# Kernel optimization log

Measured on AMD Instinct MI355X. Metric: run time of the kernel, lower is better.

## Reference

```python
import jax, jax.numpy as jnp
import numpy as np

N, E, D, S, H, L = 20000, 320000, 128, 16, 4, 64


def _ln(x, g, b):
    m = x.mean(-1, keepdims=True)
    v = jnp.mean((x - m) ** 2, -1, keepdims=True)
    return (x - m) / jnp.sqrt(v + 1e-6) * g + b


def _mlp3(x, w1, b1, g1, be1, w2, b2, g2, be2, w3, b3):
    h = jax.nn.silu(_ln(x @ w1 + b1, g1, be1))
    h = jax.nn.silu(_ln(h @ w2 + b2, g2, be2))
    return h @ w3 + b3


def _seg_softmax(a, idx, n):
    # torch_geometric.utils.softmax: per-destination-group stable softmax
    m = jax.ops.segment_max(a, idx, num_segments=n)
    m = jnp.where(jnp.isfinite(m), m, 0.0)
    e = jnp.exp(a - m[idx])
    s = jax.ops.segment_sum(e, idx, num_segments=n)
    return e / (s[idx] + 1e-16)


def setup_inputs() -> dict:
    key = jax.random.key(0)
    ks = jax.random.split(key, 32)
    rn = lambda k, sh, sc=1.0: jax.random.normal(k, sh, dtype=jnp.float32) * sc
    li = lambda k, fi, fo: rn(k, (fi, fo), 1.0 / np.sqrt(fi))
    z = lambda n_: jnp.zeros((n_,), jnp.float32)
    o = lambda n_: jnp.ones((n_,), jnp.float32)
    inp = {
        'node_in': rn(ks[0], (N, D)),
        'node_embed': rn(ks[1], (N, D)),
        'edge_sh': rn(ks[2], (E, S)),
        'edge_length_embedding': rn(ks[3], (E, L)),
        'edge_src': jax.random.randint(ks[4], (E,), 0, N, dtype=jnp.int32),
        'edge_dst': jax.random.randint(ks[5], (E,), 0, N, dtype=jnp.int32),
        'batch': jnp.zeros((N,), jnp.int32),
        'pre_lin_w': li(ks[6], 2 * D + L, D),
        'tp2_w1': li(ks[7], L, 64), 'tp2_b1': z(64),
        'tp2_w2': li(ks[8], 64, H * S), 'tp2_b2': z(H * S),
        'a_w1': li(ks[9], L, 64), 'a_b1': z(64), 'a_g1': o(64), 'a_be1': z(64),
        'a_w2': li(ks[10], 64, 64), 'a_b2': z(64), 'a_g2': o(64), 'a_be2': z(64),
        'a_w3': li(ks[11], 64, H), 'a_b3': z(H),
        'lin_w': li(ks[12], D * H, D),
        'lin_edge_w': li(ks[13], D * H, 64),
        's_w1': li(ks[14], 64, 64), 's_b1': z(64), 's_g1': o(64), 's_be1': z(64),
        's_w2': li(ks[15], 64, 64), 's_b2': z(64), 's_g2': o(64), 's_be2': z(64),
        's_w3': li(ks[16], 64, 32), 's_b3': z(32),
    }
    return inp


def reference(node_in, node_embed, edge_sh, edge_length_embedding, edge_src, edge_dst, batch,
              pre_lin_w, tp2_w1, tp2_b1, tp2_w2, tp2_b2,
              a_w1, a_b1, a_g1, a_be1, a_w2, a_b2, a_g2, a_be2, a_w3, a_b3,
              lin_w, lin_edge_w,
              s_w1, s_b1, s_g1, s_be1, s_w2, s_b2, s_g2, s_be2, s_w3, s_b3):
    e = edge_length_embedding.shape[0]
    n = node_in.shape[0]
    # gather + pre_lin
    msg = jnp.concatenate([node_in[edge_src], node_in[edge_dst], edge_length_embedding], -1) @ pre_lin_w  # [E,D]
    # EquiConv tp2: channelwise TP with radial-MLP per-edge per-(head,sh) weights
    radial = jax.nn.silu(edge_length_embedding @ tp2_w1 + tp2_b1) @ tp2_w2 + tp2_b2  # [E,H*S]
    scal = jnp.einsum('ehs,es->eh', radial.reshape(e, H, S), edge_sh)  # [E,H]
    value = msg[:, None, :] * scal[:, :, None]  # [E,H,D]
    alpha = _mlp3(edge_length_embedding, a_w1, a_b1, a_g1, a_be1, a_w2, a_b2, a_g2, a_be2, a_w3, a_b3)  # [E,H]
    edge_out = value * alpha[:, :, None]  # [E,H,D]
    edge_scalar = _mlp3(edge_out.reshape(e, -1) @ lin_edge_w,
                        s_w1, s_b1, s_g1, s_be1, s_w2, s_b2, s_g2, s_be2, s_w3, s_b3)  # [E,32]
    asm = _seg_softmax(alpha, edge_dst, n)  # [E,H]
    node_fea = jax.ops.segment_sum(value * asm[:, :, None], edge_dst, num_segments=n)  # [N,H,D]
    node_out = node_fea.reshape(n, -1) @ lin_w  # [N,D]
    return node_out, edge_scalar
```

## Files before the change

### kernel.cpp

```cpp
#include <hip/hip_runtime.h>

#define NN 20000
#define EE 320000
#define WTOT 27648

typedef unsigned short u16;
typedef unsigned int u32;
typedef __attribute__((ext_vector_type(8))) short bf16x8;
typedef __attribute__((ext_vector_type(8))) _Float16 f16x8;
typedef __attribute__((ext_vector_type(4))) float f32x4;

__device__ __forceinline__ float bf2f(u16 u){
  union { u32 i; float f; } v; v.i = ((u32)u) << 16; return v.f;
}
__device__ __forceinline__ u16 f2bf(float f){
  union { float f; u32 i; } v; v.f = f;
  u32 i = v.i;
  return (u16)((i + 0x7FFFu + ((i >> 16) & 1u)) >> 16);
}
__device__ __forceinline__ u16 f2h(float f){
  union { _Float16 h[2]; u32 u; } v; v.h[0] = (_Float16)f;
  return (u16)(v.u & 0xFFFF);
}
__device__ __forceinline__ float h2f(u16 u){
  union { u32 i; _Float16 h[2]; } v; v.i = u; return (float)v.h[0];
}
__device__ __forceinline__ u32 packh2(float a, float b){
  return ((u32)f2h(b) << 16) | (u32)f2h(a);
}

__global__ __launch_bounds__(256) void k_prep(
    const float* __restrict__ plw, const float* __restrict__ lew,
    const float* __restrict__ lw,
    u16* __restrict__ Bt1, u16* __restrict__ Bt2, u16* __restrict__ Bt3)
{
  int i = blockIdx.x * 256 + threadIdx.x;
  if (i < 128*320) {
    int n = i / 320, k = i % 320;
    Bt1[i] = f2h(plw[k*128 + n]);
  }
  int j = i - 128*320;
  if (j >= 0 && j < 256*128) {
    int n = j / 128, k = j % 128;
    int h = n >> 6, c = n & 63;
    Bt2[j] = f2h(lew[(h*128 + k)*64 + c]);
  }
  int l = i - 128*320 - 256*128;
  if (l >= 0 && l < 128*512) {
    int n = l / 512, k = l % 512;
    Bt3[l] = f2bf(lw[k*128 + n]);
  }
}

__global__ __launch_bounds__(256) void k_prep2(
    const float* __restrict__ aw1, const float* __restrict__ aw2, const float* __restrict__ aw3,
    const float* __restrict__ rw1, const float* __restrict__ rw2,
    const float* __restrict__ sw1, const float* __restrict__ sw2, const float* __restrict__ sw3,
    u16* __restrict__ W)
{
  int i = blockIdx.x * 256 + threadIdx.x;
  if (i >= WTOT) return;
  float v = 0.f;
  int j = i;
  if (j < 8192)      { int n = j >> 6, k = j & 63;
                       v = (n < 64) ? aw1[k*64 + n] : rw1[k*64 + (n - 64)]; }
  else if ((j -= 8192) < 4096) { int n = j >> 6, k = j & 63; v = aw2[k*64 + n]; }
  else if ((j -= 4096) < 1024) { int n = j >> 6, k = j & 63; v = (n < 4) ? aw3[k*4 + n] : 0.f; }
  else if ((j -= 1024) < 4096) { int n = j >> 6, k = j & 63; v = rw2[k*64 + n]; }
  else if ((j -= 4096) < 4096) { int n = j >> 6, k = j & 63; v = sw1[k*64 + n]; }
  else if ((j -= 4096) < 4096) { int n = j >> 6, k = j & 63; v = sw2[k*64 + n]; }
  else               { j -= 4096; int n = j >> 6, k = j & 63; v = sw3[k*32 + n]; }
  W[i] = f2h(v);
}

__global__ __launch_bounds__(256) void k_prep3(
    const float* __restrict__ elen, const float* __restrict__ node_in,
    u16* __restrict__ elen16, u16* __restrict__ node16)
{
  size_t i = (size_t)blockIdx.x * 256 + threadIdx.x;
  const size_t n1 = (size_t)EE * 64 / 8;
  const float* src;
  u16* dst;
  if (i < n1) { src = elen + i*8; dst = elen16 + i*8; }
  else {
    size_t j = i - n1;
    if (j >= (size_t)NN * 128 / 8) return;
    src = node_in + j*8; dst = node16 + j*8;
  }
  float4 a = ((const float4*)src)[0];
  float4 b = ((const float4*)src)[1];
  uint4 vh;
  vh.x = packh2(a.x, a.y); vh.y = packh2(a.z, a.w);
  vh.z = packh2(b.x, b.y); vh.w = packh2(b.z, b.w);
  *(uint4*)dst = vh;
}

__global__ __launch_bounds__(256) void k_zero(int* __restrict__ counts){
  int i = blockIdx.x * 256 + threadIdx.x;
  if (i < NN) counts[i] = 0;
}
__global__ __launch_bounds__(256) void k_count(const int* __restrict__ edst, int* __restrict__ counts){
  int e = blockIdx.x * 256 + threadIdx.x;
  if (e < EE) atomicAdd(&counts[edst[e]], 1);
}
__global__ __launch_bounds__(1024) void k_scan(const int* __restrict__ counts,
                                               int* __restrict__ offs, int* __restrict__ cursor){
  __shared__ int part[1024];
  int t = threadIdx.x;
  int c0 = t * 20, c1 = c0 + 20; if (c1 > NN) c1 = NN; if (c0 > NN) c0 = NN;
  int s = 0;
  for (int i = c0; i < c1; ++i) s += counts[i];
  part[t] = s;
  __syncthreads();
  if (t == 0) {
    int run = 0;
    for (int i = 0; i < 1024; ++i) { int v = part[i]; part[i] = run; run += v; }
    offs[NN] = run;
  }
  __syncthreads();
  int run = part[t];
  for (int i = c0; i < c1; ++i) { offs[i] = run; cursor[i] = run; run += counts[i]; }
}
__global__ __launch_bounds__(256) void k_fill(const int* __restrict__ edst,
                                              int* __restrict__ cursor, int* __restrict__ eids){
  int e = blockIdx.x * 256 + threadIdx.x;
  if (e < EE) { int p = atomicAdd(&cursor[edst[e]], 1); eids[p] = e; }
}
__global__ __launch_bounds__(256) void k_sort(const int* __restrict__ offs, int* __restrict__ eids){
  int n = blockIdx.x * 256 + threadIdx.x;
  if (n >= NN) return;
  int b = offs[n], e = offs[n+1];
  for (int i = b + 1; i < e; ++i) {
    int v = eids[i]; int j = i - 1;
    while (j >= b && eids[j] > v) { eids[j+1] = eids[j]; --j; }
    eids[j+1] = v;
  }
}

template<int NI>
__device__ __forceinline__ void gemm16_lds(const u16 (*X)[72], int wrow, int lane,
                                           const u16* __restrict__ B, f32x4 acc[2][4])
{
  const int fr = lane & 15, fc = lane >> 4;
  #pragma unroll
  for (int mi = 0; mi < 2; ++mi)
    #pragma unroll
    for (int ni = 0; ni < NI; ++ni)
      acc[mi][ni] = (f32x4){0.f, 0.f, 0.f, 0.f};
  #pragma unroll
  for (int kk = 0; kk < 2; ++kk) {
    f16x8 a0 = *(const f16x8*)&X[wrow + fr][kk*32 + fc*8];
    f16x8 a1 = *(const f16x8*)&X[wrow + 16 + fr][kk*32 + fc*8];
    #pragma unroll
    for (int ni = 0; ni < NI; ++ni) {
      f16x8 b = *(const f16x8*)(B + (size_t)(ni*16 + fr)*64 + kk*32 + fc*8);
      acc[0][ni] = __builtin_amdgcn_mfma_f32_16x16x32_f16(a0, b, acc[0][ni], 0, 0, 0);
      acc[1][ni] = __builtin_amdgcn_mfma_f32_16x16x32_f16(a1, b, acc[1][ni], 0, 0, 0);
    }
  }
}

template<int NI>
__device__ __forceinline__ void gemm16_lds1(const u16 (*X)[72], int wrow, int lane,
                                            const u16* __restrict__ B, f32x4 acc[4])
{
  const int fr = lane & 15, fc = lane >> 4;
  #pragma unroll
  for (int ni = 0; ni < NI; ++ni) acc[ni] = (f32x4){0.f, 0.f, 0.f, 0.f};
  #pragma unroll
  for (int kk = 0; kk < 2; ++kk) {
    f16x8 a = *(const f16x8*)&X[wrow + fr][kk*32 + fc*8];
    #pragma unroll
    for (int ni = 0; ni < NI; ++ni) {
      f16x8 b = *(const f16x8*)(B + (size_t)(ni*16 + fr)*64 + kk*32 + fc*8);
      acc[ni] = __builtin_amdgcn_mfma_f32_16x16x32_f16(a, b, acc[ni], 0, 0, 0);
    }
  }
}

__device__ __forceinline__ void gemm16_glb8(const u16* __restrict__ X, int row0, int lane,
                                            const u16* __restrict__ B, f32x4 acc[2][8])
{
  const int fr = lane & 15, fc = lane >> 4;
  #pragma unroll
  for (int mi = 0; mi < 2; ++mi)
    #pragma unroll
    for (int ni = 0; ni < 8; ++ni)
      acc[mi][ni] = (f32x4){0.f, 0.f, 0.f, 0.f};
  #pragma unroll
  for (int kk = 0; kk < 2; ++kk) {
    f16x8 a0 = *(const f16x8*)(X + (size_t)(row0 + fr)*64 + kk*32 + fc*8);
    f16x8 a1 = *(const f16x8*)(X + (size_t)(row0 + 16 + fr)*64 + kk*32 + fc*8);
    #pragma unroll
    for (int ni = 0; ni < 8; ++ni) {
      f16x8 b = *(const f16x8*)(B + (size_t)(ni*16 + fr)*64 + kk*32 + fc*8);
      acc[0][ni] = __builtin_amdgcn_mfma_f32_16x16x32_f16(a0, b, acc[0][ni], 0, 0, 0);
      acc[1][ni] = __builtin_amdgcn_mfma_f32_16x16x32_f16(a1, b, acc[1][ni], 0, 0, 0);
    }
  }
}

template<bool LN>
__device__ __forceinline__ void act_store16(f32x4 acc[2][4],
    const float* __restrict__ b, const float* __restrict__ g, const float* __restrict__ be,
    u16 (*H)[72], int wrow, int lane)
{
  const int fr = lane & 15, fc = lane >> 4;
  float bv[4], gv[4], bev[4];
  #pragma unroll
  for (int ni = 0; ni < 4; ++ni) {
    bv[ni] = b[ni*16 + fr];
    if (LN) { gv[ni] = g[ni*16 + fr]; bev[ni] = be[ni*16 + fr]; }
  }
  #pragma unroll
  for (int mi = 0; mi < 2; ++mi)
    #pragma unroll
    for (int j = 0; j < 4; ++j) {
      int r = wrow + mi*16 + fc*4 + j;
      float x[4];
      #pragma unroll
      for (int ni = 0; ni < 4; ++ni) x[ni] = acc[mi][ni][j] + bv[ni];
      if (LN) {
        float s  = x[0] + x[1] + x[2] + x[3];
        float s2 = x[0]*x[0] + x[1]*x[1] + x[2]*x[2] + x[3]*x[3];
        #pragma unroll
        for (int off = 1; off < 16; off <<= 1) {
          s  += __shfl_xor(s,  off);
          s2 += __shfl_xor(s2, off);
        }
        float mu  = s * (1.f/64.f);
        float var = s2 * (1.f/64.f) - mu*mu;
        float rs  = rsqrtf(var + 1e-6f);
        #pragma unroll
        for (int ni = 0; ni < 4; ++ni) x[ni] = (x[ni] - mu)*rs*gv[ni] + bev[ni];
      }
      #pragma unroll
      for (int ni = 0; ni < 4; ++ni) {
        float y = x[ni];
        y = y / (1.f + __expf(-y));
        H[r][ni*16 + fr] = f2h(y);
      }
    }
}

template<bool LN>
__device__ __forceinline__ void act_store16_1(f32x4 acc[4],
    const float* __restrict__ b, const float* __restrict__ g, const float* __restrict__ be,
    u16 (*H)[72], int wrow, int lane)
{
  const int fr = lane & 15, fc = lane >> 4;
  float bv[4], gv[4], bev[4];
  #pragma unroll
  for (int ni = 0; ni < 4; ++ni) {
    bv[ni] = b[ni*16 + fr];
    if (LN) { gv[ni] = g[ni*16 + fr]; bev[ni] = be[ni*16 + fr]; }
  }
  #pragma unroll
  for (int j = 0; j < 4; ++j) {
    int r = wrow + fc*4 + j;
    float x[4];
    #pragma unroll
    for (int ni = 0; ni < 4; ++ni) x[ni] = acc[ni][j] + bv[ni];
    if (LN) {
      float s  = x[0] + x[1] + x[2] + x[3];
      float s2 = x[0]*x[0] + x[1]*x[1] + x[2]*x[2] + x[3]*x[3];
      #pragma unroll
      for (int off = 1; off < 16; off <<= 1) {
        s  += __shfl_xor(s,  off);
        s2 += __shfl_xor(s2, off);
      }
      float mu  = s * (1.f/64.f);
      float var = s2 * (1.f/64.f) - mu*mu;
      float rs  = rsqrtf(var + 1e-6f);
      #pragma unroll
      for (int ni = 0; ni < 4; ++ni) x[ni] = (x[ni] - mu)*rs*gv[ni] + bev[ni];
    }
    #pragma unroll
    for (int ni = 0; ni < 4; ++ni) {
      float y = x[ni];
      y = y / (1.f + __expf(-y));
      H[r][ni*16 + fr] = f2h(y);
    }
  }
}

union ESmem {
  struct { u16 Ha[128][72]; u16 Hr[128][72]; } m;
  struct { u16 As[128][40]; u16 Bs[128][40]; } g;
};
__global__ __launch_bounds__(256, 4) void k_edge1(
  const u16* __restrict__ elen16, const float* __restrict__ esh,
  const u16* __restrict__ Wm,
  const float* __restrict__ ab1, const float* __restrict__ ag1, const float* __restrict__ abe1,
  const float* __restrict__ ab2, const float* __restrict__ ag2, const float* __restrict__ abe2,
  const float* __restrict__ ab3,
  const float* __restrict__ tb1, const float* __restrict__ tb2,
  float* __restrict__ alpha_g, float* __restrict__ scal_g, float* __restrict__ cbuf_g,
  const u16* __restrict__ node16,
  const int* __restrict__ esrc, const int* __restrict__ edst,
  const u16* __restrict__ Bt1, u16* __restrict__ msgb)
{
  __shared__ ESmem u;
  __shared__ float aS[128][4];
  const u16* Wc1 = Wm;
  const u16* Wa2 = Wm + 8192;
  const u16* Wa3 = Wm + 12288;
  const u16* Wr2 = Wm + 13312;
  const int tid = threadIdx.x;
  const int wave = tid >> 6, lane = tid & 63;
  const int fr = lane & 15, fc = lane >> 4;
  const int e0 = blockIdx.x * 128;
  {
    const int wrow = wave * 32;
    {
      f32x4 acc8[2][8];
      gemm16_glb8(elen16, e0 + wrow, lane, Wc1, acc8);
      float bva[4], gva[4], beva[4], bvr[4];
      #pragma unroll
      for (int ni = 0; ni < 4; ++ni) {
        bva[ni] = ab1[ni*16 + fr]; gva[ni] = ag1[ni*16 + fr]; beva[ni] = abe1[ni*16 + fr];
        bvr[ni] = tb1[ni*16 + fr];
      }
      #pragma unroll
      for (int mi = 0; mi < 2; ++mi)
        #pragma unroll
        for (int j = 0; j < 4; ++j) {
          int r = wrow + mi*16 + fc*4 + j;
          float xa[4], xr[4];
          #pragma unroll
          for (int ni = 0; ni < 4; ++ni) {
            xa[ni] = acc8[mi][ni][j] + bva[ni];
            xr[ni] = acc8[mi][ni+4][j] + bvr[ni];
          }
          float s  = xa[0] + xa[1] + xa[2] + xa[3];
          float s2 = xa[0]*xa[0] + xa[1]*xa[1] + xa[2]*xa[2] + xa[3]*xa[3];
          #pragma unroll
          for (int off = 1; off < 16; off <<= 1) {
            s  += __shfl_xor(s,  off);
            s2 += __shfl_xor(s2, off);
          }
          float mu  = s * (1.f/64.f);
          float var = s2 * (1.f/64.f) - mu*mu;
          float rs  = rsqrtf(var + 1e-6f);
          #pragma unroll
          for (int ni = 0; ni < 4; ++ni) {
            float y = (xa[ni] - mu)*rs*gva[ni] + beva[ni];
            y = y / (1.f + __expf(-y));
            u.m.Ha[r][ni*16 + fr] = f2h(y);
            float z = xr[ni];
            z = z / (1.f + __expf(-z));
            u.m.Hr[r][ni*16 + fr] = f2h(z);
          }
        }
    }
    f32x4 acc[2][4];
    gemm16_lds<4>(u.m.Ha, wrow, lane, Wa2, acc);
    act_store16<true>(acc, ab2, ag2, abe2, u.m.Ha, wrow, lane);
    gemm16_lds<1>(u.m.Ha, wrow, lane, Wa3, acc);
    {
      float bv = (fr < 4) ? ab3[fr] : 0.f;
      #pragma unroll
      for (int mi = 0; mi < 2; ++mi)
        #pragma unroll
        for (int j = 0; j < 4; ++j) {
          int r = wrow + mi*16 + fc*4 + j;
          float v = acc[mi][0][j] + bv;
          if (fr < 4) {
            alpha_g[(size_t)(e0 + r)*4 + fr] = v;
            aS[r][fr] = v;
          }
        }
    }
    gemm16_lds<4>(u.m.Hr, wrow, lane, Wr2, acc);
    {
      float bv[4];
      #pragma unroll
      for (int ni = 0; ni < 4; ++ni) bv[ni] = tb2[ni*16 + fr];
      #pragma unroll
      for (int mi = 0; mi < 2; ++mi)
        #pragma unroll
        for (int j = 0; j < 4; ++j) {
          int r = wrow + mi*16 + fc*4 + j;
          float shv = esh[(size_t)(e0 + r)*16 + fr];
          float sc[4];
          #pragma unroll
          for (int ni = 0; ni < 4; ++ni) {
            float t = (acc[mi][ni][j] + bv[ni]) * shv;
            #pragma unroll
            for (int off = 1; off < 16; off <<= 1) t += __shfl_xor(t, off);
            sc[ni] = t;
          }
          if (fr == 0) {
            float4 sv; sv.x = sc[0]; sv.y = sc[1]; sv.z = sc[2]; sv.w = sc[3];
            *(float4*)(scal_g + (size_t)(e0 + r)*4) = sv;
            float4 cv;
            cv.x = sc[0]*aS[r][0]; cv.y = sc[1]*aS[r][1];
            cv.z = sc[2]*aS[r][2]; cv.w = sc[3]*aS[r][3];
            *(float4*)(cbuf_g + (size_t)(e0 + r)*4) = cv;
          }
        }
    }
  }
  __syncthreads();
  {
    const int wr = (wave >> 1) * 64, wc = (wave & 1) * 64;
    f32x4 acc[4][4] = {};
    const int r = tid >> 1, half = tid & 1;
    const int e = e0 + r;
    const int s_idx = esrc[e], d_idx = edst[e];
    for (int k0 = 0; k0 < 320; k0 += 32) {
      const int kk = k0 + half * 16;
      const u16* ap;
      if (kk < 128)      ap = node16 + (size_t)s_idx*128 + kk;
      else if (kk < 256) ap = node16 + (size_t)d_idx*128 + (kk - 128);
      else               ap = elen16 + (size_t)e*64 + (kk - 256);
      uint4* asp = (uint4*)&u.g.As[r][half*16];
      asp[0] = ((const uint4*)ap)[0];
      asp[1] = ((const uint4*)ap)[1];
      const uint4* bp = (const uint4*)(Bt1 + (size_t)r*320 + kk);
      *(uint4*)&u.g.Bs[r][half*16]     = bp[0];
      *(uint4*)&u.g.Bs[r][half*16 + 8] = bp[1];
      __syncthreads();
      f16x8 a[4], b[4];
      #pragma unroll
      for (int mi = 0; mi < 4; ++mi) a[mi] = *(const f16x8*)&u.g.As[wr + mi*16 + fr][fc*8];
      #pragma unroll
      for (int ni = 0; ni < 4; ++ni) b[ni] = *(const f16x8*)&u.g.Bs[wc + ni*16 + fr][fc*8];
      #pragma unroll
      for (int mi = 0; mi < 4; ++mi)
        #pragma unroll
        for (int ni = 0; ni < 4; ++ni)
          acc[mi][ni] = __builtin_amdgcn_mfma_f32_16x16x32_f16(a[mi], b[ni], acc[mi][ni], 0, 0, 0);
      __syncthreads();
    }
    #pragma unroll
    for (int mi = 0; mi < 4; ++mi)
      #pragma unroll
      for (int j = 0; j < 4; ++j) {
        int row = wr + mi*16 + fc*4 + j;
        size_t base = (size_t)(e0 + row)*128 + wc + fr;
        #pragma unroll
        for (int ni = 0; ni < 4; ++ni)
          msgb[base + ni*16] = f2h(acc[mi][ni][j]);
      }
  }
}

__global__ __launch_bounds__(256, 4) void g2s(
    const u16* __restrict__ msgb, const u16* __restrict__ Bt2,
    const float* __restrict__ cbuf, const u16* __restrict__ Wm,
    const float* __restrict__ b1, const float* __restrict__ g1, const float* __restrict__ be1,
    const float* __restrict__ b2, const float* __restrict__ g2, const float* __restrict__ be2,
    const float* __restrict__ b3,
    float* __restrict__ oute)
{
  __shared__ u16 Bs[256][40];
  __shared__ u16 X[64][72];
  __shared__ float cS[64][4];
  const u16* Ws1 = Wm + 17408;
  const u16* Ws2 = Wm + 21504;
  const u16* Ws3 = Wm + 25600;
  const int tid = threadIdx.x, wave = tid >> 6, lane = tid & 63;
  const int e0 = blockIdx.x * 64;
  const int fr = lane & 15, fc = lane >> 4;
  const int wrow = wave * 16;
  cS[tid >> 2][tid & 3] = cbuf[(size_t)e0*4 + tid];
  f16x8 a[4];
  {
    const u16* arow = msgb + (size_t)(e0 + wrow + fr)*128 + fc*8;
    #pragma unroll
    for (int k0i = 0; k0i < 4; ++k0i) a[k0i] = *(const f16x8*)(arow + k0i*32);
  }
  f32x4 acc[16];
  #pragma unroll
  for (int ni = 0; ni < 16; ++ni) acc[ni] = (f32x4){0.f, 0.f, 0.f, 0.f};
  const u16* bsrc = Bt2 + (size_t)tid*128;
  #pragma unroll
  for (int k0i = 0; k0i < 4; ++k0i) {
    {
      const uint4* bp = (const uint4*)(bsrc + k0i*32);
      *(uint4*)&Bs[tid][0]  = bp[0];
      *(uint4*)&Bs[tid][8]  = bp[1];
      *(uint4*)&Bs[tid][16] = bp[2];
      *(uint4*)&Bs[tid][24] = bp[3];
    }
    __syncthreads();
    #pragma unroll
    for (int ni = 0; ni < 16; ++ni) {
      f16x8 b = *(const f16x8*)&Bs[ni*16 + fr][fc*8];
      acc[ni] = __builtin_amdgcn_mfma_f32_16x16x32_f16(a[k0i], b, acc[ni], 0, 0, 0);
    }
    __syncthreads();
  }
  #pragma unroll
  for (int j = 0; j < 4; ++j) {
    int r = wrow + fc*4 + j;
    float c0 = cS[r][0], c1 = cS[r][1], c2 = cS[r][2], c3 = cS[r][3];
    #pragma unroll
    for (int m = 0; m < 4; ++m) {
      float y = c0*acc[m][j] + c1*acc[4+m][j] + c2*acc[8+m][j] + c3*acc[12+m][j];
      X[r][m*16 + fr] = f2h(y);
    }
  }
  f32x4 sa[4];
  gemm16_lds1<4>(X, wrow, lane, Ws1, sa);
  act_store16_1<true>(sa, b1, g1, be1, X, wrow, lane);
  gemm16_lds1<4>(X, wrow, lane, Ws2, sa);
  act_store16_1<true>(sa, b2, g2, be2, X, wrow, lane);
  gemm16_lds1<2>(X, wrow, lane, Ws3, sa);
  {
    float bv0 = b3[fr], bv1 = b3[16 + fr];
    #pragma unroll
    for (int j = 0; j < 4; ++j) {
      int r = wrow + fc*4 + j;
      oute[(size_t)(e0 + r)*32 + fr]      = sa[0][j] + bv0;
      oute[(size_t)(e0 + r)*32 + 16 + fr] = sa[1][j] + bv1;
    }
  }
}

__global__ __launch_bounds__(256) void k_node(
  const int* __restrict__ offs, const int* __restrict__ eids,
  const float* __restrict__ alpha, const float* __restrict__ scal,
  const u16* __restrict__ msgb, u16* __restrict__ nfb)
{
  const int w = threadIdx.x >> 6, lane = threadIdx.x & 63;
  const int n = blockIdx.x * 4 + w;
  const int beg = offs[n], end = offs[n+1];
  float m0=-3e38f, m1=-3e38f, m2=-3e38f, m3=-3e38f;
  for (int i = beg + lane; i < end; i += 64) {
    int eid = eids[i];
    float4 a = *(const float4*)(alpha + (size_t)eid*4);
    m0 = fmaxf(m0, a.x); m1 = fmaxf(m1, a.y);
    m2 = fmaxf(m2, a.z); m3 = fmaxf(m3, a.w);
  }
  #pragma unroll
  for (int off = 1; off < 64; off <<= 1) {
    m0 = fmaxf(m0, __shfl_xor(m0, off));
    m1 = fmaxf(m1, __shfl_xor(m1, off));
    m2 = fmaxf(m2, __shfl_xor(m2, off));
    m3 = fmaxf(m3, __shfl_xor(m3, off));
  }
  float se0=0.f, se1=0.f, se2=0.f, se3=0.f;
  float f00=0.f, f01=0.f, f10=0.f, f11=0.f, f20=0.f, f21=0.f, f30=0.f, f31=0.f;
  for (int i = beg; i < end; ++i) {
    int eid = eids[i];
    float4 a = *(const float4*)(alpha + (size_t)eid*4);
    float4 s = *(const float4*)(scal + (size_t)eid*4);
    float e0 = __expf(a.x - m0), e1 = __expf(a.y - m1);
    float e2 = __expf(a.z - m2), e3 = __expf(a.w - m3);
    se0 += e0; se1 += e1; se2 += e2; se3 += e3;
    float w0 = e0*s.x, w1 = e1*s.y, w2 = e2*s.z, w3 = e3*s.w;
    float v0 = h2f(msgb[(size_t)eid*128 + lane]);
    float v1 = h2f(msgb[(size_t)eid*128 + 64 + lane]);
    f00 = fmaf(w0, v0, f00); f01 = fmaf(w0, v1, f01);
    f10 = fmaf(w1, v0, f10); f11 = fmaf(w1, v1, f11);
    f20 = fmaf(w2, v0, f20); f21 = fmaf(w2, v1, f21);
    f30 = fmaf(w3, v0, f30); f31 = fmaf(w3, v1, f31);
  }
  float i0 = 1.f/(se0 + 1e-16f), i1 = 1.f/(se1 + 1e-16f);
  float i2 = 1.f/(se2 + 1e-16f), i3 = 1.f/(se3 + 1e-16f);
  size_t b = (size_t)n * 512;
  nfb[b + 0*128 + lane]      = f2bf(f00*i0);
  nfb[b + 0*128 + 64 + lane] = f2bf(f01*i0);
  nfb[b + 1*128 + lane]      = f2bf(f10*i1);
  nfb[b + 1*128 + 64 + lane] = f2bf(f11*i1);
  nfb[b + 2*128 + lane]      = f2bf(f20*i2);
  nfb[b + 2*128 + 64 + lane] = f2bf(f21*i2);
  nfb[b + 3*128 + lane]      = f2bf(f30*i3);
  nfb[b + 3*128 + 64 + lane] = f2bf(f31*i3);
}

__global__ __launch_bounds__(256) void g10_out(
    const u16* __restrict__ nfb, const u16* __restrict__ Bt3,
    float* __restrict__ out)
{
  __shared__ u16 As[128][40];
  __shared__ u16 Bs[128][40];
  const int tid = threadIdx.x;
  const int n0 = blockIdx.x * 128;
  const int wave = tid >> 6, lane = tid & 63;
  const int wr = (wave >> 1) * 64, wc = (wave & 1) * 64;
  const int fr = lane & 15, fc = lane >> 4;
  f32x4 acc[4][4] = {};
  const int r = tid >> 1, half = tid & 1;
  const int n = n0 + r;
  for (int k0 = 0; k0 < 512; k0 += 32) {
    uint4 z; z.x=0; z.y=0; z.z=0; z.w=0;
    uint4 v0 = z, v1 = z;
    if (n < NN) {
      const uint4* apv = (const uint4*)(nfb + (size_t)n*512 + k0 + half*16);
      v0 = apv[0]; v1 = apv[1];
    }
    *(uint4*)&As[r][half*16]     = v0;
    *(uint4*)&As[r][half*16 + 8] = v1;
    const uint4* bp = (const uint4*)(Bt3 + (size_t)r*512 + k0 + half*16);
    *(uint4*)&Bs[r][half*16]     = bp[0];
    *(uint4*)&Bs[r][half*16 + 8] = bp[1];
    __syncthreads();
    bf16x8 a[4], b[4];
    #pragma unroll
    for (int mi = 0; mi < 4; ++mi) a[mi] = *(const bf16x8*)&As[wr + mi*16 + fr][fc*8];
    #pragma unroll
    for (int ni = 0; ni < 4; ++ni) b[ni] = *(const bf16x8*)&Bs[wc + ni*16 + fr][fc*8];
    #pragma unroll
    for (int mi = 0; mi < 4; ++mi)
      #pragma unroll
      for (int ni = 0; ni < 4; ++ni)
        acc[mi][ni] = __builtin_amdgcn_mfma_f32_16x16x32_bf16(a[mi], b[ni], acc[mi][ni], 0, 0, 0);
    __syncthreads();
  }
  #pragma unroll
  for (int mi = 0; mi < 4; ++mi)
    #pragma unroll
    for (int j = 0; j < 4; ++j) {
      int rowg = n0 + wr + mi*16 + fc*4 + j;
      if (rowg < NN) {
        size_t base = (size_t)rowg*128 + wc + fr;
        #pragma unroll
        for (int ni = 0; ni < 4; ++ni)
          out[base + ni*16] = acc[mi][ni][j];
      }
    }
}

extern "C" void kernel_launch(void* const* d_in, const int* in_sizes, int n_in,
                              void* d_out, int out_size, void* d_ws, size_t ws_size,
                              hipStream_t stream)
{
  const float* node_in    = (const float*)d_in[0];
  const float* edge_sh    = (const float*)d_in[2];
  const float* elen       = (const float*)d_in[3];
  const int*   esrc       = (const int*)d_in[4];
  const int*   edst       = (const int*)d_in[5];
  const float* pre_lin_w  = (const float*)d_in[7];
  const float* tp2_w1     = (const float*)d_in[8];
  const float* tp2_b1     = (const float*)d_in[9];
  const float* tp2_w2     = (const float*)d_in[10];
  const float* tp2_b2     = (const float*)d_in[11];
  const float* a_w1  = (const float*)d_in[12];
  const float* a_b1  = (const float*)d_in[13];
  const float* a_g1  = (const float*)d_in[14];
  const float* a_be1 = (const float*)d_in[15];
  const float* a_w2  = (const float*)d_in[16];
  const float* a_b2  = (const float*)d_in[17];
  const float* a_g2  = (const float*)d_in[18];
  const float* a_be2 = (const float*)d_in[19];
  const float* a_w3  = (const float*)d_in[20];
  const float* a_b3  = (const float*)d_in[21];
  const float* lin_w      = (const float*)d_in[22];
  const float* lin_edge_w = (const float*)d_in[23];
  const float* s_w1  = (const float*)d_in[24];
  const float* s_b1  = (const float*)d_in[25];
  const float* s_g1  = (const float*)d_in[26];
  const float* s_be1 = (const float*)d_in[27];
  const float* s_w2  = (const float*)d_in[28];
  const float* s_b2  = (const float*)d_in[29];
  const float* s_g2  = (const float*)d_in[30];
  const float* s_be2 = (const float*)d_in[31];
  const float* s_w3  = (const float*)d_in[32];
  const float* s_b3  = (const float*)d_in[33];

  float* out_node = (float*)d_out;
  float* out_edge = out_node + (size_t)NN * 128;

  char* ws = (char*)d_ws;
  size_t off = 0;
  auto take = [&](size_t bytes) -> char* {
    char* p = ws + off;
    off = (off + bytes + 255) & ~(size_t)255;
    return p;
  };
  u16*   msgb   = (u16*)take((size_t)EE * 128 * 2);
  u16*   elen16 = (u16*)take((size_t)EE * 64 * 2);
  u16*   node16 = (u16*)take((size_t)NN * 128 * 2);
  u16*   nfb    = (u16*)take((size_t)NN * 512 * 2);
  float* alpha  = (float*)take((size_t)EE * 4 * 4);
  float* scal   = (float*)take((size_t)EE * 4 * 4);
  float* cbuf   = (float*)take((size_t)EE * 4 * 4);
  int*   counts = (int*)take((size_t)NN * 4);
  int*   offs   = (int*)take((size_t)(NN + 1) * 4);
  int*   cursor = (int*)take((size_t)NN * 4);
  int*   eids   = (int*)take((size_t)EE * 4);
  u16*   Bt1    = (u16*)take((size_t)128 * 320 * 2);
  u16*   Bt2    = (u16*)take((size_t)256 * 128 * 2);
  u16*   Bt3    = (u16*)take((size_t)128 * 512 * 2);
  u16*   Wmlp   = (u16*)take((size_t)WTOT * 2);

  const int prep3_thr = EE*64/8 + NN*128/8;
  k_prep<<<544, 256, 0, stream>>>(pre_lin_w, lin_edge_w, lin_w, Bt1, Bt2, Bt3);
  k_prep2<<<(WTOT + 255)/256, 256, 0, stream>>>(a_w1, a_w2, a_w3, tp2_w1, tp2_w2,
                                                s_w1, s_w2, s_w3, Wmlp);
  k_prep3<<<(prep3_thr + 255)/256, 256, 0, stream>>>(elen, node_in, elen16, node16);
  k_zero<<<(NN + 255)/256, 256, 0, stream>>>(counts);
  k_count<<<EE/256, 256, 0, stream>>>(edst, counts);
  k_scan<<<1, 1024, 0, stream>>>(counts, offs, cursor);
  k_fill<<<EE/256, 256, 0, stream>>>(edst, cursor, eids);
  k_sort<<<(NN + 255)/256, 256, 0, stream>>>(offs, eids);
  k_edge1<<<EE/128, 256, 0, stream>>>(elen16, edge_sh, Wmlp,
                                      a_b1, a_g1, a_be1, a_b2, a_g2, a_be2, a_b3,
                                      tp2_b1, tp2_b2, alpha, scal, cbuf,
                                      node16, esrc, edst, Bt1, msgb);
  g2s<<<EE/64, 256, 0, stream>>>(msgb, Bt2, cbuf, Wmlp,
                                 s_b1, s_g1, s_be1, s_b2, s_g2, s_be2, s_b3, out_edge);
  k_node<<<NN/4, 256, 0, stream>>>(offs, eids, alpha, scal, msgb, nfb);
  g10_out<<<(NN + 127)/128, 256, 0, stream>>>(nfb, Bt3, out_node);
}
```

Before: 470.1 us.

## Merge prep kernels, parallelize scan and per-node sort, use rcp-based SiLU

```diff
diff --git a/kernel.cpp b/kernel.cpp
--- a/kernel.cpp
+++ b/kernel.cpp
@@ -3,6 +3,7 @@
 #define NN 20000
 #define EE 320000
 #define WTOT 27648
+#define P3N (EE*64/8 + NN*128/8)
 
 typedef unsigned short u16;
 typedef unsigned int u32;
@@ -28,77 +29,74 @@
 __device__ __forceinline__ u32 packh2(float a, float b){
   return ((u32)f2h(b) << 16) | (u32)f2h(a);
 }
-
-__global__ __launch_bounds__(256) void k_prep(
+__device__ __forceinline__ float fsilu(float y){
+  return y * __builtin_amdgcn_rcpf(1.f + __expf(-y));
+}
+
+__global__ __launch_bounds__(256) void k_prep_all(
+    const float* __restrict__ elen, const float* __restrict__ node_in,
+    u16* __restrict__ elen16, u16* __restrict__ node16,
+    int* __restrict__ counts,
     const float* __restrict__ plw, const float* __restrict__ lew,
     const float* __restrict__ lw,
-    u16* __restrict__ Bt1, u16* __restrict__ Bt2, u16* __restrict__ Bt3)
-{
-  int i = blockIdx.x * 256 + threadIdx.x;
-  if (i < 128*320) {
-    int n = i / 320, k = i % 320;
-    Bt1[i] = f2h(plw[k*128 + n]);
-  }
-  int j = i - 128*320;
-  if (j >= 0 && j < 256*128) {
-    int n = j / 128, k = j % 128;
-    int h = n >> 6, c = n & 63;
-    Bt2[j] = f2h(lew[(h*128 + k)*64 + c]);
-  }
-  int l = i - 128*320 - 256*128;
-  if (l >= 0 && l < 128*512) {
-    int n = l / 512, k = l % 512;
-    Bt3[l] = f2bf(lw[k*128 + n]);
-  }
-}
-
-__global__ __launch_bounds__(256) void k_prep2(
+    u16* __restrict__ Bt1, u16* __restrict__ Bt2, u16* __restrict__ Bt3,
     const float* __restrict__ aw1, const float* __restrict__ aw2, const float* __restrict__ aw3,
     const float* __restrict__ rw1, const float* __restrict__ rw2,
     const float* __restrict__ sw1, const float* __restrict__ sw2, const float* __restrict__ sw3,
     u16* __restrict__ W)
 {
-  int i = blockIdx.x * 256 + threadIdx.x;
-  if (i >= WTOT) return;
-  float v = 0.f;
-  int j = i;
-  if (j < 8192)      { int n = j >> 6, k = j & 63;
-                       v = (n < 64) ? aw1[k*64 + n] : rw1[k*64 + (n - 64)]; }
-  else if ((j -= 8192) < 4096) { int n = j >> 6, k = j & 63; v = aw2[k*64 + n]; }
-  else if ((j -= 4096) < 1024) { int n = j >> 6, k = j & 63; v = (n < 4) ? aw3[k*4 + n] : 0.f; }
-  else if ((j -= 1024) < 4096) { int n = j >> 6, k = j & 63; v = rw2[k*64 + n]; }
-  else if ((j -= 4096) < 4096) { int n = j >> 6, k = j & 63; v = sw1[k*64 + n]; }
-  else if ((j -= 4096) < 4096) { int n = j >> 6, k = j & 63; v = sw2[k*64 + n]; }
-  else               { j -= 4096; int n = j >> 6, k = j & 63; v = sw3[k*32 + n]; }
-  W[i] = f2h(v);
-}
-
-__global__ __launch_bounds__(256) void k_prep3(
-    const float* __restrict__ elen, const float* __restrict__ node_in,
-    u16* __restrict__ elen16, u16* __restrict__ node16)
-{
-  size_t i = (size_t)blockIdx.x * 256 + threadIdx.x;
-  const size_t n1 = (size_t)EE * 64 / 8;
-  const float* src;
-  u16* dst;
-  if (i < n1) { src = elen + i*8; dst = elen16 + i*8; }
-  else {
-    size_t j = i - n1;
-    if (j >= (size_t)NN * 128 / 8) return;
-    src = node_in + j*8; dst = node16 + j*8;
-  }
-  float4 a = ((const float4*)src)[0];
-  float4 b = ((const float4*)src)[1];
-  uint4 vh;
-  vh.x = packh2(a.x, a.y); vh.y = packh2(a.z, a.w);
-  vh.z = packh2(b.x, b.y); vh.w = packh2(b.z, b.w);
-  *(uint4*)dst = vh;
-}
-
-__global__ __launch_bounds__(256) void k_zero(int* __restrict__ counts){
-  int i = blockIdx.x * 256 + threadIdx.x;
-  if (i < NN) counts[i] = 0;
-}
+  size_t gi = (size_t)blockIdx.x * 256 + threadIdx.x;
+  if (gi < (size_t)P3N) {
+    const size_t n1 = (size_t)EE * 64 / 8;
+    const float* src;
+    u16* dst;
+    if (gi < n1) { src = elen + gi*8; dst = elen16 + gi*8; }
+    else { size_t j = gi - n1; src = node_in + j*8; dst = node16 + j*8; }
+    float4 a = ((const float4*)src)[0];
+    float4 b = ((const float4*)src)[1];
+    uint4 vh;
+    vh.x = packh2(a.x, a.y); vh.y = packh2(a.z, a.w);
+    vh.z = packh2(b.x, b.y); vh.w = packh2(b.z, b.w);
+    *(uint4*)dst = vh;
+    return;
+  }
+  long j = (long)gi - P3N;
+  if (j < NN) { counts[j] = 0; return; }
+  j -= NN;
+  if (j < 128*320) {
+    int n = (int)j / 320, k = (int)j % 320;
+    Bt1[j] = f2h(plw[k*128 + n]);
+    return;
+  }
+  j -= 128*320;
+  if (j < 256*128) {
+    int n = (int)j / 128, k = (int)j % 128;
+    int h = n >> 6, c = n & 63;
+    Bt2[j] = f2h(lew[(h*128 + k)*64 + c]);
+    return;
+  }
+  j -= 256*128;
+  if (j < 128*512) {
+    int n = (int)j / 512, k = (int)j % 512;
+    Bt3[j] = f2bf(lw[k*128 + n]);
+    return;
+  }
+  j -= 128*512;
+  if (j < WTOT) {
+    float v = 0.f;
+    long i = j;
+    if (i < 8192)      { int n = i >> 6, k = i & 63;
+                         v = (n < 64) ? aw1[k*64 + n] : rw1[k*64 + (n - 64)]; }
+    else if ((i -= 8192) < 4096) { int n = i >> 6, k = i & 63; v = aw2[k*64 + n]; }
+    else if ((i -= 4096) < 1024) { int n = i >> 6, k = i & 63; v = (n < 4) ? aw3[k*4 + n] : 0.f; }
+    else if ((i -= 1024) < 4096) { int n = i >> 6, k = i & 63; v = rw2[k*64 + n]; }
+    else if ((i -= 4096) < 4096) { int n = i >> 6, k = i & 63; v = sw1[k*64 + n]; }
+    else if ((i -= 4096) < 4096) { int n = i >> 6, k = i & 63; v = sw2[k*64 + n]; }
+    else               { i -= 4096; int n = i >> 6, k = i & 63; v = sw3[k*32 + n]; }
+    W[j] = f2h(v);
+  }
+}
+
 __global__ __launch_bounds__(256) void k_count(const int* __restrict__ edst, int* __restrict__ counts){
   int e = blockIdx.x * 256 + threadIdx.x;
   if (e < EE) atomicAdd(&counts[edst[e]], 1);
@@ -112,13 +110,17 @@
   for (int i = c0; i < c1; ++i) s += counts[i];
   part[t] = s;
   __syncthreads();
-  if (t == 0) {
-    int run = 0;
-    for (int i = 0; i < 1024; ++i) { int v = part[i]; part[i] = run; run += v; }
-    offs[NN] = run;
-  }
-  __syncthreads();
-  int run = part[t];
+  int acc = s;
+  #pragma unroll
+  for (int d = 1; d < 1024; d <<= 1) {
+    int v = (t >= d) ? part[t - d] : 0;
+    __syncthreads();
+    acc += v;
+    part[t] = acc;
+    __syncthreads();
+  }
+  if (t == 1023) offs[NN] = acc;
+  int run = acc - s;
   for (int i = c0; i < c1; ++i) { offs[i] = run; cursor[i] = run; run += counts[i]; }
 }
 __global__ __launch_bounds__(256) void k_fill(const int* __restrict__ edst,
@@ -126,14 +128,26 @@
   int e = blockIdx.x * 256 + threadIdx.x;
   if (e < EE) { int p = atomicAdd(&cursor[edst[e]], 1); eids[p] = e; }
 }
-__global__ __launch_bounds__(256) void k_sort(const int* __restrict__ offs, int* __restrict__ eids){
-  int n = blockIdx.x * 256 + threadIdx.x;
+__global__ __launch_bounds__(256) void k_sort2(const int* __restrict__ offs, int* __restrict__ eids){
+  int w = threadIdx.x >> 6, lane = threadIdx.x & 63;
+  int n = blockIdx.x * 4 + w;
   if (n >= NN) return;
-  int b = offs[n], e = offs[n+1];
-  for (int i = b + 1; i < e; ++i) {
-    int v = eids[i]; int j = i - 1;
-    while (j >= b && eids[j] > v) { eids[j+1] = eids[j]; --j; }
-    eids[j+1] = v;
+  int beg = offs[n], end = offs[n+1], deg = end - beg;
+  if (deg <= 1) return;
+  if (deg <= 64) {
+    int v = (lane < deg) ? eids[beg + lane] : 0x7fffffff;
+    int rank = 0;
+    for (int j = 0; j < deg; ++j) {
+      int u = __shfl(v, j);
+      rank += (u < v) ? 1 : 0;
+    }
+    if (lane < deg) eids[beg + rank] = v;
+  } else if (lane == 0) {
+    for (int i = beg + 1; i < end; ++i) {
+      int v = eids[i]; int j = i - 1;
+      while (j >= beg && eids[j] > v) { eids[j+1] = eids[j]; --j; }
+      eids[j+1] = v;
+    }
   }
 }
 
@@ -235,11 +249,8 @@
         for (int ni = 0; ni < 4; ++ni) x[ni] = (x[ni] - mu)*rs*gv[ni] + bev[ni];
       }
       #pragma unroll
-      for (int ni = 0; ni < 4; ++ni) {
-        float y = x[ni];
-        y = y / (1.f + __expf(-y));
-        H[r][ni*16 + fr] = f2h(y);
-      }
+      for (int ni = 0; ni < 4; ++ni)
+        H[r][ni*16 + fr] = f2h(fsilu(x[ni]));
     }
 }
 
@@ -276,11 +287,8 @@
       for (int ni = 0; ni < 4; ++ni) x[ni] = (x[ni] - mu)*rs*gv[ni] + bev[ni];
     }
     #pragma unroll
-    for (int ni = 0; ni < 4; ++ni) {
-      float y = x[ni];
-      y = y / (1.f + __expf(-y));
-      H[r][ni*16 + fr] = f2h(y);
-    }
+    for (int ni = 0; ni < 4; ++ni)
+      H[r][ni*16 + fr] = f2h(fsilu(x[ni]));
   }
 }
 
@@ -345,11 +353,8 @@
           #pragma unroll
           for (int ni = 0; ni < 4; ++ni) {
             float y = (xa[ni] - mu)*rs*gva[ni] + beva[ni];
-            y = y / (1.f + __expf(-y));
-            u.m.Ha[r][ni*16 + fr] = f2h(y);
-            float z = xr[ni];
-            z = z / (1.f + __expf(-z));
-            u.m.Hr[r][ni*16 + fr] = f2h(z);
+            u.m.Ha[r][ni*16 + fr] = f2h(fsilu(y));
+            u.m.Hr[r][ni*16 + fr] = f2h(fsilu(xr[ni]));
           }
         }
     }
@@ -687,16 +692,15 @@
   u16*   Bt3    = (u16*)take((size_t)128 * 512 * 2);
   u16*   Wmlp   = (u16*)take((size_t)WTOT * 2);
 
-  const int prep3_thr = EE*64/8 + NN*128/8;
-  k_prep<<<544, 256, 0, stream>>>(pre_lin_w, lin_edge_w, lin_w, Bt1, Bt2, Bt3);
-  k_prep2<<<(WTOT + 255)/256, 256, 0, stream>>>(a_w1, a_w2, a_w3, tp2_w1, tp2_w2,
-                                                s_w1, s_w2, s_w3, Wmlp);
-  k_prep3<<<(prep3_thr + 255)/256, 256, 0, stream>>>(elen, node_in, elen16, node16);
-  k_zero<<<(NN + 255)/256, 256, 0, stream>>>(counts);
+  const long prep_total = (long)P3N + NN + 128*320 + 256*128 + 128*512 + WTOT;
+  k_prep_all<<<(int)((prep_total + 255)/256), 256, 0, stream>>>(
+      elen, node_in, elen16, node16, counts,
+      pre_lin_w, lin_edge_w, lin_w, Bt1, Bt2, Bt3,
+      a_w1, a_w2, a_w3, tp2_w1, tp2_w2, s_w1, s_w2, s_w3, Wmlp);
   k_count<<<EE/256, 256, 0, stream>>>(edst, counts);
   k_scan<<<1, 1024, 0, stream>>>(counts, offs, cursor);
   k_fill<<<EE/256, 256, 0, stream>>>(edst, cursor, eids);
-  k_sort<<<(NN + 255)/256, 256, 0, stream>>>(offs, eids);
+  k_sort2<<<NN/4, 256, 0, stream>>>(offs, eids);
   k_edge1<<<EE/128, 256, 0, stream>>>(elen16, edge_sh, Wmlp,
                                       a_b1, a_g1, a_be1, a_b2, a_g2, a_be2, a_b3,
                                       tp2_b1, tp2_b2, alpha, scal, cbuf,
```

Result: faster. 400.1 us (-14.9%).
